# Kernel optimization log

Measured on AMD Instinct MI355X. Metric: run time of the kernel, lower is better.

The kernel has to match this reference:

```python
import jax, jax.numpy as jnp
import numpy as np

N, D, H, HD, R, K, TM = 32768, 128, 2, 64, 2, 32, 2
E_EDGES, M_MOTIFS, NG = 262144, 131072, 32
EPS = 1e-5
BETA_MAX = 5.0
GRAD_CLIP = 1.0
STATE_CLIP = 10.0
DAMPING = 1.0

def _isp(x):
    # inverse softplus of init values (params stored pre-softplus)
    return float(np.log(np.expm1(x)))

LAM2_RAW, LAM3_RAW, LAMM_RAW = _isp(1.0), _isp(0.5), _isp(1.0)
B2_RAW, B3_RAW, BM_RAW = _isp(1.0), _isp(1.0), _isp(1.0)


def layernorm(x, g, b):
    mu = x.mean(-1, keepdims=True)
    v = ((x - mu) ** 2).mean(-1, keepdims=True)
    return g * (x - mu) * jax.lax.rsqrt(v + EPS) + b


def seg_lse(s, seg, n, beta):
    # tempered logsumexp over segments: (1/beta) log sum_j exp(beta*s_j); s:[items,H] -> [n,H]
    sb = beta * s
    m = jax.ops.segment_max(sb, seg, num_segments=n)
    m = jnp.where(jnp.isfinite(m), m, 0.0)
    z = jax.ops.segment_sum(jnp.exp(sb - m[seg]), seg, num_segments=n)
    return jnp.where(z > 0, (m + jnp.log(jnp.maximum(z, 1e-30))) / beta, 0.0)


def energy(X, a_2, ln_gamma, ln_beta, W_Q2, W_K2, W_Q3, W_K3, T_tau, W_Qm, W_Km, B_mem,
           c_2, u_2, c_3, u_3, v_3, t_tau, batch):
    sp = jax.nn.softplus
    lam2, lam3, lamm = sp(LAM2_RAW), sp(LAM3_RAW), sp(LAMM_RAW)
    b2 = jnp.minimum(sp(B2_RAW), BETA_MAX)
    b3 = jnp.minimum(sp(B3_RAW), BETA_MAX)
    bm = jnp.minimum(sp(BM_RAW), BETA_MAX)
    G = layernorm(X, ln_gamma, ln_beta)
    # pairwise Q2/K2 term over edges (c_2 <- u_2) with learned per-edge bias a_2
    Q2 = jnp.einsum('nd,hzd->nhz', G, W_Q2)  # [N,H,HD]
    K2 = jnp.einsum('nd,hzd->nhz', G, W_K2)
    s2 = jnp.einsum('ehz,ehz->eh', Q2[c_2], K2[u_2]) / np.sqrt(HD) + a_2  # [E,H]
    e_pair = -lam2 * seg_lse(s2, c_2, N, b2).sum(-1)  # [N]
    # rank-R bilinear motif term over (c_3,u_3,v_3) with type embedding T_tau
    Q3 = jnp.einsum('nd,hzd->nhz', G, W_Q3).reshape(N, H, R, HD)
    K3 = jnp.einsum('nd,hzd->nhz', G, W_K3).reshape(N, H, R, HD)
    qk = jnp.einsum('mhrz,mhrz->mhr', Q3[c_3], K3[u_3])
    tv = jnp.einsum('mhrz,mhrz->mhr', T_tau[t_tau], K3[v_3])
    s3 = (qk * tv).sum(-1) / HD  # [M,H]
    e_motif = -lam3 * seg_lse(s3, c_3, N, b3).sum(-1)
    # K-slot memory term
    Qm = jnp.einsum('nd,hzd->nhz', G, W_Qm)
    Km = jnp.einsum('kd,hzd->hkz', B_mem, W_Km)
    sm = jnp.einsum('nhz,hkz->nhk', Qm, Km) / np.sqrt(HD)
    e_mem = -(lamm / bm) * jax.nn.logsumexp(bm * sm, axis=-1).sum(-1)
    e_node = 0.5 * (X * X).sum(-1) + e_pair + e_motif + e_mem
    return jax.ops.segment_sum(e_node, batch, num_segments=NG)  # per-graph energy [NG]


def setup_inputs() -> dict:
    key = jax.random.key(0)
    ks = jax.random.split(key, 16)
    inp = {}
    inp['X'] = jax.random.normal(ks[0], (N, D), jnp.float32)
    inp['c_2'] = jax.random.randint(ks[1], (E_EDGES,), 0, N)
    inp['u_2'] = jax.random.randint(ks[2], (E_EDGES,), 0, N)
    inp['c_3'] = jax.random.randint(ks[3], (M_MOTIFS,), 0, N)
    inp['u_3'] = jax.random.randint(ks[4], (M_MOTIFS,), 0, N)
    inp['v_3'] = jax.random.randint(ks[5], (M_MOTIFS,), 0, N)
    inp['t_tau'] = jax.random.randint(ks[6], (M_MOTIFS,), 0, TM)
    inp['batch'] = jnp.sort(jax.random.randint(ks[7], (N,), 0, NG))
    inp['a_2'] = 0.1 * jax.random.normal(ks[8], (E_EDGES, H), jnp.float32)
    inp['step_size'] = jnp.full((1,), 0.1, jnp.float32)
    inp['ln_gamma'] = jnp.ones((D,), jnp.float32)
    inp['ln_beta'] = jnp.zeros((D,), jnp.float32)
    s = 1.0 / np.sqrt(D)
    inp['W_Q2'] = s * jax.random.normal(ks[9], (H, HD, D), jnp.float32)
    inp['W_K2'] = s * jax.random.normal(ks[10], (H, HD, D), jnp.float32)
    inp['W_Q3'] = 0.5 * s * jax.random.normal(ks[11], (H, R * HD, D), jnp.float32)
    inp['W_K3'] = 0.5 * s * jax.random.normal(ks[12], (H, R * HD, D), jnp.float32)
    inp['T_tau'] = 0.02 * jax.random.normal(ks[13], (TM, H, R, HD), jnp.float32)
    inp['W_Qm'] = 0.5 * s * jax.random.normal(ks[14], (H, HD, D), jnp.float32)
    inp['W_Km'] = 0.5 * s * jax.random.normal(ks[15], (H, HD, D), jnp.float32)
    inp['B_mem'] = s * jax.random.normal(jax.random.fold_in(key, 99), (K, D), jnp.float32)
    return inp


def reference(X, c_2, u_2, c_3, u_3, v_3, t_tau, batch, a_2, step_size,
              ln_gamma, ln_beta, W_Q2, W_K2, W_Q3, W_K3, T_tau, W_Qm, W_Km, B_mem):
    Eg, vjp = jax.vjp(
        lambda Xv: energy(Xv, a_2, ln_gamma, ln_beta, W_Q2, W_K2, W_Q3, W_K3, T_tau,
                          W_Qm, W_Km, B_mem, c_2, u_2, c_3, u_3, v_3, t_tau, batch), X)
    gX, = vjp(jnp.ones_like(Eg))
    gnorm = jnp.linalg.norm(gX, axis=-1, keepdims=True)
    gX = gX * (GRAD_CLIP / jnp.maximum(gnorm, GRAD_CLIP))
    X_next = X - step_size[0] * DAMPING * gX
    snorm = jnp.linalg.norm(X_next, axis=-1, keepdims=True)
    X_next = X_next * (STATE_CLIP / jnp.maximum(snorm, STATE_CLIP))
    return X_next, Eg
```

## Files before the change

kernel.cpp:

```cpp
#include <hip/hip_runtime.h>
#include <hip/hip_bf16.h>
#include <math.h>

typedef __hip_bfloat16 bf16;
typedef short bf16x8 __attribute__((ext_vector_type(8)));
typedef float f32x4 __attribute__((ext_vector_type(4)));

#define N_NODES 32768
#define D_DIM 128
#define E_EDG 262144
#define M_MOT 131072
#define NG_G 32
#define F_TOT 832

__device__ __forceinline__ float wsum64(float v){
#pragma unroll
  for (int o = 32; o > 0; o >>= 1) v += __shfl_xor(v, o, 64);
  return v;
}
__device__ __forceinline__ float hsum32(float v){
#pragma unroll
  for (int o = 16; o > 0; o >>= 1) v += __shfl_xor(v, o, 64);
  return v;
}
__device__ __forceinline__ float hmax32(float v){
#pragma unroll
  for (int o = 16; o > 0; o >>= 1) v = fmaxf(v, __shfl_xor(v, o, 64));
  return v;
}
__device__ __forceinline__ float hsum16(float v){
#pragma unroll
  for (int o = 8; o > 0; o >>= 1) v += __shfl_xor(v, o, 64);
  return v;
}
__device__ __forceinline__ float hsum8(float v){
#pragma unroll
  for (int o = 4; o > 0; o >>= 1) v += __shfl_xor(v, o, 64);
  return v;
}
__device__ __forceinline__ float bsum128(float v, float* scr, int t){
  float s = wsum64(v);
  if ((t & 63) == 0) scr[t >> 6] = s;
  __syncthreads();
  float r = scr[0] + scr[1];
  __syncthreads();
  return r;
}
__device__ __forceinline__ float bflo(unsigned u){ return __uint_as_float(u << 16); }
__device__ __forceinline__ float bfhi(unsigned u){ return __uint_as_float(u & 0xffff0000u); }
__device__ __forceinline__ unsigned packbf(float x, float y){
  bf16 a = __float2bfloat16(x), b = __float2bfloat16(y);
  unsigned short ua = *(unsigned short*)&a, ub = *(unsigned short*)&b;
  return (unsigned)ua | ((unsigned)ub << 16);
}
__device__ __forceinline__ void unpk8(uint4 p, float* f){
  f[0] = bflo(p.x); f[1] = bfhi(p.x); f[2] = bflo(p.y); f[3] = bfhi(p.y);
  f[4] = bflo(p.z); f[5] = bfhi(p.z); f[6] = bflo(p.w); f[7] = bfhi(p.w);
}

__global__ __launch_bounds__(256) void k_phaseA(
    const int* c2, const int* u2, const int* c3, const int* u3, const int* v3,
    const float* wq2, const float* wk2, const float* wq3, const float* wk3,
    const float* wqm, const float* wkm, const float* bmem, const float* Ttau,
    int* cnt, float* Wcat, bf16* Ttb, float* Mprod){
  __shared__ float KmL[64];
  int b = blockIdx.x, t = threadIdx.x;
  if (b < 1024){
    int i = b * 256 + t;
    atomicAdd(&cnt[c2[i]], 1);
    atomicAdd(&cnt[N_NODES + u2[i]], 1);
    if (i < M_MOT){
      atomicAdd(&cnt[2 * N_NODES + c3[i]], 1);
      atomicAdd(&cnt[3 * N_NODES + u3[i]], 1);
      atomicAdd(&cnt[4 * N_NODES + v3[i]], 1);
    }
  } else if (b < 1440){
    int idx = (b - 1024) * 256 + t;
    if (idx < 768 * D_DIM){
      int f = idx / D_DIM, d = idx - f * D_DIM;
      const float* src; int fr;
      if      (f < 128){ src = wq2; fr = f; }
      else if (f < 256){ src = wk2; fr = f - 128; }
      else if (f < 512){ src = wq3; fr = f - 256; }
      else             { src = wk3; fr = f - 512; }
      Wcat[f * D_DIM + d] = src[fr * D_DIM + d];
    } else {
      int j = idx - 768 * D_DIM;
      Ttb[j] = __float2bfloat16(Ttau[j]);
    }
  } else {
    int hk = b - 1440;
    int h = hk >> 5, k = hk & 31;
    if (t < 64){
      const float* wrow = wkm + (size_t)(h * 64 + t) * D_DIM;
      const float* brow = bmem + k * D_DIM;
      float acc = 0.f;
      for (int d = 0; d < D_DIM; d++) acc += wrow[d] * brow[d];
      KmL[t] = acc;
    }
    __syncthreads();
    if (t < 128){
      const float* w = wqm + (size_t)(h * 64) * 128 + t;
      float acc = 0.f;
      for (int z = 0; z < 64; z++) acc += w[z * 128] * KmL[z];
      Mprod[t * 64 + hk] = acc;
    }
  }
}

__global__ __launch_bounds__(1024) void k_phaseB(
    int* cntcur, int* off,
    const float* X, const float* gamma, const float* beta,
    bf16* Gb, float* mu, float* rstd, float* e_node,
    const float* Wcat, const float* Mprod, bf16* wfF, bf16* wfB){
  __shared__ int sd[1024];
  int b = blockIdx.x, t = threadIdx.x;
  if (b < 5){
    int a = b;
    int* c = cntcur + a * N_NODES;
    int* o = off + a * (N_NODES + 1);
    int loc[32];
    int sum = 0;
#pragma unroll
    for (int j = 0; j < 32; j++){ loc[j] = sum; sum += c[t * 32 + j]; }
    sd[t] = sum;
    __syncthreads();
    for (int s = 1; s < 1024; s <<= 1){
      int v = (t >= s) ? sd[t - s] : 0;
      __syncthreads();
      sd[t] += v;
      __syncthreads();
    }
    int excl = sd[t] - sum;
#pragma unroll
    for (int j = 0; j < 32; j++){
      int val = excl + loc[j];
      o[t * 32 + j] = val;
      c[t * 32 + j] = val;
    }
    if (t == 1023) o[N_NODES] = sd[1023];
  } else if (b < 2053){
    int wv = t >> 6, l = t & 63;
    int n = (b - 5) * 16 + wv;
    float2 x2 = ((const float2*)(X + (size_t)n * 128))[l];
    float sumx = wsum64(x2.x + x2.y);
    float sumxx = wsum64(x2.x * x2.x + x2.y * x2.y);
    float m = sumx * (1.0f / 128.0f);
    float var = sumxx * (1.0f / 128.0f) - m * m;
    float rs = rsqrtf(var + 1e-5f);
    float2 gg = ((const float2*)gamma)[l];
    float2 bb = ((const float2*)beta)[l];
    ((unsigned*)(Gb + (size_t)n * 128))[l] =
        packbf(gg.x * (x2.x - m) * rs + bb.x, gg.y * (x2.y - m) * rs + bb.y);
    if (l == 0){ mu[n] = m; rstd[n] = rs; e_node[n] = 0.5f * sumxx; }
  } else {
    int idx = (b - 2053) * 1024 + t;
    int j = idx & 7, lane = (idx >> 3) & 63, tt = idx >> 9;
    {
      int tn = tt >> 2, kt = tt & 3;
      int f = tn * 16 + (lane & 15), d = kt * 32 + (lane >> 4) * 8 + j;
      float v = (f < 768) ? Wcat[f * 128 + d] : 0.125f * Mprod[d * 64 + (f - 768)];
      wfF[idx] = __float2bfloat16(v);
    }
    {
      int td = tt / 26, tf = tt - td * 26;
      int f = tf * 32 + (lane >> 4) * 8 + j, d = td * 16 + (lane & 15);
      float v = (f < 768) ? Wcat[f * 128 + d] : -0.125f * Mprod[d * 64 + (f - 768)];
      wfB[idx] = __float2bfloat16(v);
    }
  }
}

__global__ __launch_bounds__(256) void k_phaseC(
    const bf16* Gb, const bf16* wfF, bf16* P,
    const int* c2, const int* u2, const int* c3, const int* u3, const int* v3,
    const int* tt, const float* a2, int* cur,
    uint2* lec, uint2* leu, uint2* lmc, uint2* lmu, uint2* lmv){
  int b = blockIdx.x;
  int g = b / 15, r = b - g * 15;
  if (r < 13){
    int f = g * 13 + r;
    int bx = f & 511, by = f >> 9;
    int wave = threadIdx.x >> 6, lane = threadIdx.x & 63;
    int m0 = bx * 64 + wave * 16;
    int tn0 = by * 4;
    int rw = lane & 15, quad = lane >> 4;
    const bf16* aptr = Gb + (size_t)(m0 + rw) * 128 + quad * 8;
    bf16x8 a[4];
#pragma unroll
    for (int kt = 0; kt < 4; kt++) a[kt] = *(const bf16x8*)(aptr + kt * 32);
    f32x4 acc[4];
#pragma unroll
    for (int i = 0; i < 4; i++) acc[i] = (f32x4){0.f, 0.f, 0.f, 0.f};
#pragma unroll
    for (int nf = 0; nf < 4; nf++){
      int tn = tn0 + nf;
#pragma unroll
      for (int kt = 0; kt < 4; kt++){
        bf16x8 bb = *(const bf16x8*)(wfF + (((size_t)tn * 4 + kt) * 64 + lane) * 8);
        acc[nf] = __builtin_amdgcn_mfma_f32_16x16x32_bf16(a[kt], bb, acc[nf], 0, 0, 0);
      }
    }
#pragma unroll
    for (int nf = 0; nf < 4; nf++){
      int col = (tn0 + nf) * 16 + rw;
#pragma unroll
      for (int rr = 0; rr < 4; rr++){
        int row = m0 + quad * 4 + rr;
        P[(size_t)row * F_TOT + col] = __float2bfloat16(acc[nf][rr]);
      }
    }
  } else {
    int i = (g * 2 + (r - 13)) * 256 + threadIdx.x;
    {
      int c = c2[i], u = u2[i];
      int posc = atomicAdd(&cur[c], 1);
      float2 av = *(const float2*)(a2 + (size_t)i * 2);
      lec[posc] = make_uint2((unsigned)u, packbf(av.x, av.y));
      int posu = atomicAdd(&cur[N_NODES + u], 1);
      leu[posu] = make_uint2((unsigned)c, (unsigned)posc);
    }
    if (i < M_MOT){
      int c = c3[i], u = u3[i], v = v3[i], t = tt[i];
      int posc = atomicAdd(&cur[2 * N_NODES + c], 1);
      lmc[posc] = make_uint2((unsigned)(u | (v << 16)), (unsigned)t);
      int posu = atomicAdd(&cur[3 * N_NODES + u], 1);
      lmu[posu] = make_uint2((unsigned)c, (unsigned)posc);
      int posv = atomicAdd(&cur[4 * N_NODES + v], 1);
      lmv[posv] = make_uint2((unsigned)(c | (t << 16)), (unsigned)posc);
    }
  }
}

__global__ __launch_bounds__(256) void k_fused_c(const bf16* P, const uint2* lec, const uint2* lmc,
                   const bf16* Ttb, const int* off_ec, const int* off_mc,
                   float* s2, float* rz2, float* s3, float* qkb, float* tvb, float* rz3,
                   bf16* dP, float* e_pair, float* e_mot, float* e_mem){
  int b = blockIdx.x;
  int type = b % 3, grp = b / 3;
  int wave = threadIdx.x >> 6, z = threadIdx.x & 63;
  int n = grp * 4 + wave;
  int l = z & 31, lh = z >> 5;

  if (type == 0){
    int hg = l >> 4;
    int beg = off_ec[n], end = off_ec[n + 1];
    uint2 qp = ((const uint2*)(P + (size_t)n * F_TOT))[l];
    float q0 = bflo(qp.x), q1 = bfhi(qp.x), q2 = bflo(qp.y), q3 = bfhi(qp.y);
    float a0 = 0.f, a1 = 0.f, a2 = 0.f, a3 = 0.f, zz = 0.f;
    int iters = (end - beg + 1) >> 1;
    for (int it = 0; it < iters; it++){
      int idx = beg + 2 * it + lh;
      bool valid = idx < end;
      int idc = valid ? idx : end - 1;
      uint2 pl = lec[idc];
      uint2 kp = ((const uint2*)(P + (size_t)pl.x * F_TOT + 128))[l];
      float k0 = bflo(kp.x), k1 = bfhi(kp.x), k2 = bflo(kp.y), k3 = bfhi(kp.y);
      float s = hsum16(q0 * k0 + q1 * k1 + q2 * k2 + q3 * k3) * 0.125f
              + (hg ? bfhi(pl.y) : bflo(pl.y));
      if (valid && (l & 15) == 0) s2[2 * idx + hg] = s;
      float ex = valid ? expf(s) : 0.f;
      a0 += ex * k0;  a1 += ex * k1;  a2 += ex * k2;  a3 += ex * k3;
      zz += ex;
    }
    a0 += __shfl_xor(a0, 32, 64);  a1 += __shfl_xor(a1, 32, 64);
    a2 += __shfl_xor(a2, 32, 64);  a3 += __shfl_xor(a3, 32, 64);
    zz += __shfl_xor(zz, 32, 64);
    float rz = (zz > 0.f) ? 1.0f / zz : 0.f;
    float coef = -0.125f * rz;
    if (z < 32){
      uint2 o;
      o.x = packbf(coef * a0, coef * a1);
      o.y = packbf(coef * a2, coef * a3);
      ((uint2*)(dP + (size_t)n * F_TOT))[l] = o;
      if ((l & 15) == 0) rz2[n * 2 + hg] = rz;
    }
    float eterm = (zz > 0.f) ? -logf(zz) : 0.f;
    float eo = __shfl(eterm, 16, 64);
    if (z == 0) e_pair[n] = eterm + eo;
  } else if (type == 1){
    int g = l >> 3, hg = g >> 1;
    int beg = off_mc[n], end = off_mc[n + 1];
    uint4 qp = ((const uint4*)(P + (size_t)n * F_TOT + 256))[l];
    float q[8]; unpk8(qp, q);
    float acc[8] = {0,0,0,0,0,0,0,0};
    float zz = 0.f;
    int iters = (end - beg + 1) >> 1;
    for (int it = 0; it < iters; it++){
      int idx = beg + 2 * it + lh;
      bool valid = idx < end;
      int idc = valid ? idx : end - 1;
      uint2 pl = lmc[idc];
      int u = pl.x & 0xffff, v = pl.x >> 16, t = pl.y;
      uint4 kup = ((const uint4*)(P + (size_t)u * F_TOT + 512))[l];
      uint4 kvp = ((const uint4*)(P + (size_t)v * F_TOT + 512))[l];
      uint4 tp  = ((const uint4*)(Ttb + (size_t)t * 256))[l];
      float k[8], vv[8], pt[8];
      unpk8(kup, k); unpk8(kvp, vv); unpk8(tp, pt);
      float dq = 0.f, dt = 0.f;
#pragma unroll
      for (int j = 0; j < 8; j++){ dq += q[j] * k[j]; dt += pt[j] * vv[j]; }
      float qk = hsum8(dq);
      float tv = hsum8(dt);
      if (valid && (l & 7) == 0){ qkb[(size_t)4 * idx + g] = qk; tvb[(size_t)4 * idx + g] = tv; }
      float w = qk * tv;
      float s = (w + __shfl_xor(w, 8, 64)) * (1.0f / 64.0f);
      if (valid && (l & 15) == 0) s3[2 * idx + hg] = s;
      float ex = valid ? expf(s) : 0.f;
      float et = ex * tv;
#pragma unroll
      for (int j = 0; j < 8; j++) acc[j] += et * k[j];
      zz += ex;
    }
#pragma unroll
    for (int j = 0; j < 8; j++) acc[j] += __shfl_xor(acc[j], 32, 64);
    zz += __shfl_xor(zz, 32, 64);
    float rz = (zz > 0.f) ? 1.0f / zz : 0.f;
    float coef = (-0.5f / 64.0f) * rz;
    if (z < 32){
      uint4 o;
      o.x = packbf(coef * acc[0], coef * acc[1]);
      o.y = packbf(coef * acc[2], coef * acc[3]);
      o.z = packbf(coef * acc[4], coef * acc[5]);
      o.w = packbf(coef * acc[6], coef * acc[7]);
      ((uint4*)(dP + (size_t)n * F_TOT + 256))[l] = o;
      if ((l & 15) == 0) rz3[n * 2 + hg] = rz;
    }
    float eterm = (zz > 0.f) ? -0.5f * logf(zz) : 0.f;
    float eo = __shfl(eterm, 16, 64);
    if (z == 0) e_mot[n] = eterm + eo;
  } else {
    unsigned short us = ((const unsigned short*)(P + (size_t)n * F_TOT + 768))[z];
    float s = __uint_as_float((unsigned)us << 16);
    float mx = hmax32(s);
    float ex = expf(s - mx);
    float se = hsum32(ex);
    float p = ex / se;
    bf16 pb = __float2bfloat16(p);
    ((unsigned short*)(dP + (size_t)n * F_TOT + 768))[z] = *(unsigned short*)&pb;
    float eterm = -(mx + logf(se));
    float eo = __shfl(eterm, z ^ 32, 64);
    if (z == 0) e_mem[n] = eterm + eo;
  }
}

__global__ __launch_bounds__(256) void k_phaseE(const bf16* P, const uint2* leu,
                    const uint2* lmu, const uint2* lmv, const bf16* Ttb,
                    const float* s2, const float* rz2, const float* s3, const float* rz3,
                    const float* qkb, const float* tvb,
                    const int* off_eu, const int* off_mu, const int* off_mv, bf16* dP,
                    const float* e_node, const float* e_pair, const float* e_mot,
                    const float* e_mem, const int* batch, float* Eg){
  __shared__ float eg[NG_G];
  int b = blockIdx.x;
  if (b < 128){
    int t = threadIdx.x;
    if (t < NG_G) eg[t] = 0.f;
    __syncthreads();
    int n = b * 256 + t;
    float e = e_node[n] + e_pair[n] + e_mot[n] + e_mem[n];
    atomicAdd(&eg[batch[n]], e);
    __syncthreads();
    if (t < NG_G) atomicAdd(&Eg[t], eg[t]);
    return;
  }
  int b2 = b - 128;
  int type = b2 & 1, grp = b2 >> 1;
  int wave = threadIdx.x >> 6, z = threadIdx.x & 63;
  int n = grp * 4 + wave;
  int l = z & 31, lh = z >> 5;

  if (type == 0){
    int hg = l >> 4;
    int beg = off_eu[n], end = off_eu[n + 1];
    float a0 = 0.f, a1 = 0.f, a2 = 0.f, a3 = 0.f;
    int iters = (end - beg + 1) >> 1;
    for (int it = 0; it < iters; it++){
      int idx = beg + 2 * it + lh;
      bool valid = idx < end;
      int idc = valid ? idx : end - 1;
      uint2 pl = leu[idc];
      uint2 qp = ((const uint2*)(P + (size_t)pl.x * F_TOT))[l];
      float p = valid ? expf(s2[2 * pl.y + hg]) * rz2[pl.x * 2 + hg] : 0.f;
      a0 += p * bflo(qp.x);  a1 += p * bfhi(qp.x);
      a2 += p * bflo(qp.y);  a3 += p * bfhi(qp.y);
    }
    a0 += __shfl_xor(a0, 32, 64);  a1 += __shfl_xor(a1, 32, 64);
    a2 += __shfl_xor(a2, 32, 64);  a3 += __shfl_xor(a3, 32, 64);
    if (z < 32){
      uint2 o;
      o.x = packbf(-0.125f * a0, -0.125f * a1);
      o.y = packbf(-0.125f * a2, -0.125f * a3);
      ((uint2*)(dP + (size_t)n * F_TOT + 128))[l] = o;
    }
  } else {
    int g = l >> 3, hg = g >> 1;
    float acc[8] = {0,0,0,0,0,0,0,0};
    {
      int beg = off_mu[n], end = off_mu[n + 1];
      int iters = (end - beg + 1) >> 1;
      for (int it = 0; it < iters; it++){
        int idx = beg + 2 * it + lh;
        bool valid = idx < end;
        int idc = valid ? idx : end - 1;
        uint2 pl = lmu[idc];
        unsigned c = pl.x, posc = pl.y;
        uint4 qp = ((const uint4*)(P + (size_t)c * F_TOT + 256))[l];
        float q[8]; unpk8(qp, q);
        float w = valid ? expf(s3[2 * posc + hg]) * rz3[c * 2 + hg] * tvb[(size_t)4 * posc + g] : 0.f;
#pragma unroll
        for (int j = 0; j < 8; j++) acc[j] += w * q[j];
      }
    }
    {
      int beg = off_mv[n], end = off_mv[n + 1];
      int iters = (end - beg + 1) >> 1;
      for (int it = 0; it < iters; it++){
        int idx = beg + 2 * it + lh;
        bool valid = idx < end;
        int idc = valid ? idx : end - 1;
        uint2 pl = lmv[idc];
        unsigned c = pl.x & 0xffff, t = pl.x >> 16, posc = pl.y;
        uint4 tp = ((const uint4*)(Ttb + (size_t)t * 256))[l];
        float pt[8]; unpk8(tp, pt);
        float w = valid ? expf(s3[2 * posc + hg]) * rz3[c * 2 + hg] * qkb[(size_t)4 * posc + g] : 0.f;
#pragma unroll
        for (int j = 0; j < 8; j++) acc[j] += w * pt[j];
      }
    }
#pragma unroll
    for (int j = 0; j < 8; j++) acc[j] += __shfl_xor(acc[j], 32, 64);
    const float cst = -0.5f / 64.0f;
    if (z < 32){
      uint4 o;
      o.x = packbf(cst * acc[0], cst * acc[1]);
      o.y = packbf(cst * acc[2], cst * acc[3]);
      o.z = packbf(cst * acc[4], cst * acc[5]);
      o.w = packbf(cst * acc[6], cst * acc[7]);
      ((uint4*)(dP + (size_t)n * F_TOT + 512))[l] = o;
    }
  }
}

__global__ __launch_bounds__(256) void k_bwd_mfma(const bf16* dP, const bf16* wfB, float* dG){
  int wave = threadIdx.x >> 6, lane = threadIdx.x & 63;
  int m0 = blockIdx.x * 64 + wave * 16;
  int rw = lane & 15, quad = lane >> 4;
  const bf16* aptr = dP + (size_t)(m0 + rw) * F_TOT + quad * 8;
  f32x4 acc[8];
#pragma unroll
  for (int i = 0; i < 8; i++) acc[i] = (f32x4){0.f, 0.f, 0.f, 0.f};
  for (int kt = 0; kt < 26; kt++){
    bf16x8 a = *(const bf16x8*)(aptr + kt * 32);
#pragma unroll
    for (int td = 0; td < 8; td++){
      bf16x8 b = *(const bf16x8*)(wfB + (((size_t)td * 26 + kt) * 64 + lane) * 8);
      acc[td] = __builtin_amdgcn_mfma_f32_16x16x32_bf16(a, b, acc[td], 0, 0, 0);
    }
  }
#pragma unroll
  for (int td = 0; td < 8; td++){
    int col = td * 16 + rw;
#pragma unroll
    for (int r = 0; r < 4; r++){
      int row = m0 + quad * 4 + r;
      dG[(size_t)row * 128 + col] = acc[td][r];
    }
  }
}

__global__ __launch_bounds__(128) void k_finalize(const float* X, const float* dG, const float* gamma,
                    const float* mu, const float* rstd, const float* step_p,
                    const float* Eg, float* out){
  __shared__ float scr[2];
  int n = blockIdx.x, t = threadIdx.x;
  float x = X[(size_t)n * 128 + t];
  float dg = dG[(size_t)n * 128 + t];
  float gam = gamma[t];
  float rs = rstd[n];
  float xhat = (x - mu[n]) * rs;
  float dxh = dg * gam;
  float s1 = bsum128(dxh, scr, t);
  float s2v = bsum128(dxh * xhat, scr, t);
  float dx = rs * (dxh - s1 * (1.0f / 128) - xhat * (s2v * (1.0f / 128)));
  float g = x + dx;
  float gn = sqrtf(bsum128(g * g, scr, t));
  g *= 1.0f / fmaxf(gn, 1.0f);
  float step = step_p[0];
  float xn = x - step * g;
  float sn = sqrtf(bsum128(xn * xn, scr, t));
  xn *= 10.0f / fmaxf(sn, 10.0f);
  out[(size_t)n * 128 + t] = xn;
  if (n == 0 && t < NG_G) out[(size_t)N_NODES * 128 + t] = Eg[t];
}

extern "C" void kernel_launch(void* const* d_in, const int* in_sizes, int n_in,
                              void* d_out, int out_size, void* d_ws, size_t ws_size,
                              hipStream_t stream) {
  const float* X     = (const float*)d_in[0];
  const int*  c_2    = (const int*) d_in[1];
  const int*  u_2    = (const int*) d_in[2];
  const int*  c_3    = (const int*) d_in[3];
  const int*  u_3    = (const int*) d_in[4];
  const int*  v_3    = (const int*) d_in[5];
  const int*  t_tau  = (const int*) d_in[6];
  const int*  batch  = (const int*) d_in[7];
  const float* a_2   = (const float*)d_in[8];
  const float* step_s= (const float*)d_in[9];
  const float* ln_g  = (const float*)d_in[10];
  const float* ln_b  = (const float*)d_in[11];
  const float* W_Q2  = (const float*)d_in[12];
  const float* W_K2  = (const float*)d_in[13];
  const float* W_Q3  = (const float*)d_in[14];
  const float* W_K3  = (const float*)d_in[15];
  const float* T_tau = (const float*)d_in[16];
  const float* W_Qm  = (const float*)d_in[17];
  const float* W_Km  = (const float*)d_in[18];
  const float* B_mem = (const float*)d_in[19];
  float* out = (float*)d_out;

  char* wb = (char*)d_ws;
  float* Wcat   = (float*)wb; wb += 768 * D_DIM * 4;
  float* Mprod  = (float*)wb; wb += 8192 * 4;
  float* mu     = (float*)wb; wb += N_NODES * 4;
  float* rstd   = (float*)wb; wb += N_NODES * 4;
  float* s2     = (float*)wb; wb += (size_t)E_EDG * 2 * 4;
  float* rz2    = (float*)wb; wb += N_NODES * 2 * 4;
  float* s3     = (float*)wb; wb += (size_t)M_MOT * 2 * 4;
  float* qkb    = (float*)wb; wb += (size_t)M_MOT * 4 * 4;
  float* tvb    = (float*)wb; wb += (size_t)M_MOT * 4 * 4;
  float* rz3    = (float*)wb; wb += N_NODES * 2 * 4;
  float* e_node = (float*)wb; wb += N_NODES * 4;
  float* e_pair = (float*)wb; wb += N_NODES * 4;
  float* e_mot  = (float*)wb; wb += N_NODES * 4;
  float* e_mem  = (float*)wb; wb += N_NODES * 4;
  float* Eg     = (float*)wb; wb += NG_G * 4;
  float* dG     = (float*)wb; wb += (size_t)N_NODES * D_DIM * 4;
  bf16* Gb      = (bf16*)wb;  wb += (size_t)N_NODES * D_DIM * 2;
  bf16* P       = (bf16*)wb;  wb += (size_t)N_NODES * F_TOT * 2;
  bf16* dP      = (bf16*)wb;  wb += (size_t)N_NODES * F_TOT * 2;
  bf16* wfF     = (bf16*)wb;  wb += 106496 * 2;
  bf16* wfB     = (bf16*)wb;  wb += 106496 * 2;
  bf16* Ttb     = (bf16*)wb;  wb += 8192 * 2;
  int* cntcur   = (int*)wb;   wb += 5 * N_NODES * 4;
  int* off      = (int*)wb;   wb += 5 * (N_NODES + 1) * 4;
  wb = (char*)(((size_t)wb + 15) & ~(size_t)15);
  uint2* lec    = (uint2*)wb; wb += (size_t)E_EDG * 8;
  uint2* leu    = (uint2*)wb; wb += (size_t)E_EDG * 8;
  uint2* lmc    = (uint2*)wb; wb += (size_t)M_MOT * 8;
  uint2* lmu    = (uint2*)wb; wb += (size_t)M_MOT * 8;
  uint2* lmv    = (uint2*)wb; wb += (size_t)M_MOT * 8;

  const int* off_ec = off;
  const int* off_eu = off + (N_NODES + 1);
  const int* off_mc = off + 2 * (N_NODES + 1);
  const int* off_mu = off + 3 * (N_NODES + 1);
  const int* off_mv = off + 4 * (N_NODES + 1);

  hipMemsetAsync(cntcur, 0, 5 * N_NODES * sizeof(int), stream);
  hipMemsetAsync(Eg, 0, NG_G * sizeof(float), stream);
  hipLaunchKernelGGL(k_phaseA, dim3(1504), dim3(256), 0, stream,
                     c_2, u_2, c_3, u_3, v_3, W_Q2, W_K2, W_Q3, W_K3,
                     W_Qm, W_Km, B_mem, T_tau, cntcur, Wcat, Ttb, Mprod);
  hipLaunchKernelGGL(k_phaseB, dim3(2157), dim3(1024), 0, stream,
                     cntcur, off, X, ln_g, ln_b, Gb, mu, rstd, e_node,
                     Wcat, Mprod, wfF, wfB);
  hipLaunchKernelGGL(k_phaseC, dim3(7680), dim3(256), 0, stream,
                     Gb, wfF, P, c_2, u_2, c_3, u_3, v_3, t_tau, a_2, cntcur,
                     lec, leu, lmc, lmu, lmv);
  hipLaunchKernelGGL(k_fused_c, dim3(3 * (N_NODES / 4)), dim3(256), 0, stream,
                     P, lec, lmc, Ttb, off_ec, off_mc,
                     s2, rz2, s3, qkb, tvb, rz3, dP, e_pair, e_mot, e_mem);
  hipLaunchKernelGGL(k_phaseE, dim3(128 + 2 * (N_NODES / 4)), dim3(256), 0, stream,
                     P, leu, lmu, lmv, Ttb, s2, rz2, s3, rz3, qkb, tvb,
                     off_eu, off_mu, off_mv, dP,
                     e_node, e_pair, e_mot, e_mem, batch, Eg);
  hipLaunchKernelGGL(k_bwd_mfma, dim3(N_NODES / 64), dim3(256), 0, stream, dP, wfB, dG);
  hipLaunchKernelGGL(k_finalize, dim3(N_NODES), dim3(128), 0, stream,
                     X, dG, ln_g, mu, rstd, step_s, Eg, out);
}
```

Measured before the change: 395.2 us.

## Split backward GEMM by K-tiles, overlap part with phaseE, widen pair gathers

The backward MFMA GEMM is split into two K-tile masks. Tiles whose dP rows are already final after k_fused_c are computed inside k_phaseE, running alongside the scatter work, and the remaining tiles run in a second accumulating kernel. The pair-edge loops in k_fused_c and k_phaseE now process four edges per wave with 16-byte gathers instead of two edges with 8-byte gathers. k_finalize packs four nodes per block with wave-only reductions, removing the shared-memory block syncs. The risks are the extra read-modify-write of dG in the second GEMM pass and correctness depending on the hand-coded tile masks matching which dP columns each phase writes.

Measured after the change: 459.7 us. 1.16x slower.

```diff
diff --git a/kernel.cpp b/kernel.cpp
--- a/kernel.cpp
+++ b/kernel.cpp
@@ -12,6 +12,8 @@
 #define M_MOT 131072
 #define NG_G 32
 #define F_TOT 832
+#define BWD_MASK1 0x0300FF0Fu
+#define BWD_MASK2 0x00FF00F0u
 
 __device__ __forceinline__ float wsum64(float v){
 #pragma unroll
@@ -28,23 +30,10 @@
   for (int o = 16; o > 0; o >>= 1) v = fmaxf(v, __shfl_xor(v, o, 64));
   return v;
 }
-__device__ __forceinline__ float hsum16(float v){
-#pragma unroll
-  for (int o = 8; o > 0; o >>= 1) v += __shfl_xor(v, o, 64);
-  return v;
-}
 __device__ __forceinline__ float hsum8(float v){
 #pragma unroll
   for (int o = 4; o > 0; o >>= 1) v += __shfl_xor(v, o, 64);
   return v;
-}
-__device__ __forceinline__ float bsum128(float v, float* scr, int t){
-  float s = wsum64(v);
-  if ((t & 63) == 0) scr[t >> 6] = s;
-  __syncthreads();
-  float r = scr[0] + scr[1];
-  __syncthreads();
-  return r;
 }
 __device__ __forceinline__ float bflo(unsigned u){ return __uint_as_float(u << 16); }
 __device__ __forceinline__ float bfhi(unsigned u){ return __uint_as_float(u & 0xffff0000u); }
@@ -56,6 +45,36 @@
 __device__ __forceinline__ void unpk8(uint4 p, float* f){
   f[0] = bflo(p.x); f[1] = bfhi(p.x); f[2] = bflo(p.y); f[3] = bfhi(p.y);
   f[4] = bflo(p.z); f[5] = bfhi(p.z); f[6] = bflo(p.w); f[7] = bfhi(p.w);
+}
+
+__device__ __forceinline__ void bwd_body(const bf16* dP, const bf16* wfB, float* dG,
+                                         unsigned mask, bool accum, int b, int tid){
+  int wave = tid >> 6, lane = tid & 63;
+  int m0 = b * 64 + wave * 16;
+  int rw = lane & 15, quad = lane >> 4;
+  const bf16* aptr = dP + (size_t)(m0 + rw) * F_TOT + quad * 8;
+  f32x4 acc[8];
+#pragma unroll
+  for (int i = 0; i < 8; i++) acc[i] = (f32x4){0.f, 0.f, 0.f, 0.f};
+  for (int kt = 0; kt < 26; kt++){
+    if (!((mask >> kt) & 1u)) continue;
+    bf16x8 a = *(const bf16x8*)(aptr + kt * 32);
+#pragma unroll
+    for (int td = 0; td < 8; td++){
+      bf16x8 bb = *(const bf16x8*)(wfB + (((size_t)td * 26 + kt) * 64 + lane) * 8);
+      acc[td] = __builtin_amdgcn_mfma_f32_16x16x32_bf16(a, bb, acc[td], 0, 0, 0);
+    }
+  }
+#pragma unroll
+  for (int td = 0; td < 8; td++){
+    int col = td * 16 + rw;
+#pragma unroll
+    for (int r = 0; r < 4; r++){
+      int row = m0 + quad * 4 + r;
+      if (accum) dG[(size_t)row * 128 + col] += acc[td][r];
+      else       dG[(size_t)row * 128 + col]  = acc[td][r];
+    }
+  }
 }
 
 __global__ __launch_bounds__(256) void k_phaseA(
@@ -243,46 +262,56 @@
   int l = z & 31, lh = z >> 5;
 
   if (type == 0){
-    int hg = l >> 4;
+    int q = z >> 4, l16 = z & 15, hg = l16 >> 3;
     int beg = off_ec[n], end = off_ec[n + 1];
-    uint2 qp = ((const uint2*)(P + (size_t)n * F_TOT))[l];
-    float q0 = bflo(qp.x), q1 = bfhi(qp.x), q2 = bflo(qp.y), q3 = bfhi(qp.y);
-    float a0 = 0.f, a1 = 0.f, a2 = 0.f, a3 = 0.f, zz = 0.f;
-    int iters = (end - beg + 1) >> 1;
+    uint4 qp = ((const uint4*)(P + (size_t)n * F_TOT))[l16];
+    float qv[8]; unpk8(qp, qv);
+    float acc[8] = {0,0,0,0,0,0,0,0};
+    float zz = 0.f;
+    int iters = (end - beg + 3) >> 2;
     for (int it = 0; it < iters; it++){
-      int idx = beg + 2 * it + lh;
+      int idx = beg + 4 * it + q;
       bool valid = idx < end;
       int idc = valid ? idx : end - 1;
       uint2 pl = lec[idc];
-      uint2 kp = ((const uint2*)(P + (size_t)pl.x * F_TOT + 128))[l];
-      float k0 = bflo(kp.x), k1 = bfhi(kp.x), k2 = bflo(kp.y), k3 = bfhi(kp.y);
-      float s = hsum16(q0 * k0 + q1 * k1 + q2 * k2 + q3 * k3) * 0.125f
-              + (hg ? bfhi(pl.y) : bflo(pl.y));
-      if (valid && (l & 15) == 0) s2[2 * idx + hg] = s;
+      uint4 kp = ((const uint4*)(P + (size_t)pl.x * F_TOT + 128))[l16];
+      float kv[8]; unpk8(kp, kv);
+      float d = 0.f;
+#pragma unroll
+      for (int j = 0; j < 8; j++) d += qv[j] * kv[j];
+      float s = hsum8(d) * 0.125f + (hg ? bfhi(pl.y) : bflo(pl.y));
+      if (valid && (l16 & 7) == 0) s2[2 * idx + hg] = s;
       float ex = valid ? expf(s) : 0.f;
-      a0 += ex * k0;  a1 += ex * k1;  a2 += ex * k2;  a3 += ex * k3;
+#pragma unroll
+      for (int j = 0; j < 8; j++) acc[j] += ex * kv[j];
       zz += ex;
     }
-    a0 += __shfl_xor(a0, 32, 64);  a1 += __shfl_xor(a1, 32, 64);
-    a2 += __shfl_xor(a2, 32, 64);  a3 += __shfl_xor(a3, 32, 64);
+#pragma unroll
+    for (int j = 0; j < 8; j++){
+      acc[j] += __shfl_xor(acc[j], 16, 64);
+      acc[j] += __shfl_xor(acc[j], 32, 64);
+    }
+    zz += __shfl_xor(zz, 16, 64);
     zz += __shfl_xor(zz, 32, 64);
     float rz = (zz > 0.f) ? 1.0f / zz : 0.f;
     float coef = -0.125f * rz;
-    if (z < 32){
-      uint2 o;
-      o.x = packbf(coef * a0, coef * a1);
-      o.y = packbf(coef * a2, coef * a3);
-      ((uint2*)(dP + (size_t)n * F_TOT))[l] = o;
-      if ((l & 15) == 0) rz2[n * 2 + hg] = rz;
+    if (z < 16){
+      uint4 o;
+      o.x = packbf(coef * acc[0], coef * acc[1]);
+      o.y = packbf(coef * acc[2], coef * acc[3]);
+      o.z = packbf(coef * acc[4], coef * acc[5]);
+      o.w = packbf(coef * acc[6], coef * acc[7]);
+      ((uint4*)(dP + (size_t)n * F_TOT))[l16] = o;
+      if ((l16 & 7) == 0) rz2[n * 2 + hg] = rz;
     }
     float eterm = (zz > 0.f) ? -logf(zz) : 0.f;
-    float eo = __shfl(eterm, 16, 64);
+    float eo = __shfl(eterm, 8, 64);
     if (z == 0) e_pair[n] = eterm + eo;
   } else if (type == 1){
     int g = l >> 3, hg = g >> 1;
     int beg = off_mc[n], end = off_mc[n + 1];
     uint4 qp = ((const uint4*)(P + (size_t)n * F_TOT + 256))[l];
-    float q[8]; unpk8(qp, q);
+    float qv[8]; unpk8(qp, qv);
     float acc[8] = {0,0,0,0,0,0,0,0};
     float zz = 0.f;
     int iters = (end - beg + 1) >> 1;
@@ -299,7 +328,7 @@
       unpk8(kup, k); unpk8(kvp, vv); unpk8(tp, pt);
       float dq = 0.f, dt = 0.f;
 #pragma unroll
-      for (int j = 0; j < 8; j++){ dq += q[j] * k[j]; dt += pt[j] * vv[j]; }
+      for (int j = 0; j < 8; j++){ dq += qv[j] * k[j]; dt += pt[j] * vv[j]; }
       float qk = hsum8(dq);
       float tv = hsum8(dt);
       if (valid && (l & 7) == 0){ qkb[(size_t)4 * idx + g] = qk; tvb[(size_t)4 * idx + g] = tv; }
@@ -350,48 +379,59 @@
                     const float* qkb, const float* tvb,
                     const int* off_eu, const int* off_mu, const int* off_mv, bf16* dP,
                     const float* e_node, const float* e_pair, const float* e_mot,
-                    const float* e_mem, const int* batch, float* Eg){
+                    const float* e_mem, const int* batch, float* Eg,
+                    const bf16* wfB, float* dG){
   __shared__ float eg[NG_G];
   int b = blockIdx.x;
-  if (b < 128){
+  if (b < 512){
+    bwd_body(dP, wfB, dG, BWD_MASK1, false, b, threadIdx.x);
+    return;
+  }
+  if (b < 640){
     int t = threadIdx.x;
     if (t < NG_G) eg[t] = 0.f;
     __syncthreads();
-    int n = b * 256 + t;
+    int n = (b - 512) * 256 + t;
     float e = e_node[n] + e_pair[n] + e_mot[n] + e_mem[n];
     atomicAdd(&eg[batch[n]], e);
     __syncthreads();
     if (t < NG_G) atomicAdd(&Eg[t], eg[t]);
     return;
   }
-  int b2 = b - 128;
+  int b2 = b - 640;
   int type = b2 & 1, grp = b2 >> 1;
   int wave = threadIdx.x >> 6, z = threadIdx.x & 63;
   int n = grp * 4 + wave;
   int l = z & 31, lh = z >> 5;
 
   if (type == 0){
-    int hg = l >> 4;
+    int q = z >> 4, l16 = z & 15, hg = l16 >> 3;
     int beg = off_eu[n], end = off_eu[n + 1];
-    float a0 = 0.f, a1 = 0.f, a2 = 0.f, a3 = 0.f;
-    int iters = (end - beg + 1) >> 1;
+    float acc[8] = {0,0,0,0,0,0,0,0};
+    int iters = (end - beg + 3) >> 2;
     for (int it = 0; it < iters; it++){
-      int idx = beg + 2 * it + lh;
+      int idx = beg + 4 * it + q;
       bool valid = idx < end;
       int idc = valid ? idx : end - 1;
       uint2 pl = leu[idc];
-      uint2 qp = ((const uint2*)(P + (size_t)pl.x * F_TOT))[l];
+      uint4 qp = ((const uint4*)(P + (size_t)pl.x * F_TOT))[l16];
+      float qv[8]; unpk8(qp, qv);
       float p = valid ? expf(s2[2 * pl.y + hg]) * rz2[pl.x * 2 + hg] : 0.f;
-      a0 += p * bflo(qp.x);  a1 += p * bfhi(qp.x);
-      a2 += p * bflo(qp.y);  a3 += p * bfhi(qp.y);
-    }
-    a0 += __shfl_xor(a0, 32, 64);  a1 += __shfl_xor(a1, 32, 64);
-    a2 += __shfl_xor(a2, 32, 64);  a3 += __shfl_xor(a3, 32, 64);
-    if (z < 32){
-      uint2 o;
-      o.x = packbf(-0.125f * a0, -0.125f * a1);
-      o.y = packbf(-0.125f * a2, -0.125f * a3);
-      ((uint2*)(dP + (size_t)n * F_TOT + 128))[l] = o;
+#pragma unroll
+      for (int j = 0; j < 8; j++) acc[j] += p * qv[j];
+    }
+#pragma unroll
+    for (int j = 0; j < 8; j++){
+      acc[j] += __shfl_xor(acc[j], 16, 64);
+      acc[j] += __shfl_xor(acc[j], 32, 64);
+    }
+    if (z < 16){
+      uint4 o;
+      o.x = packbf(-0.125f * acc[0], -0.125f * acc[1]);
+      o.y = packbf(-0.125f * acc[2], -0.125f * acc[3]);
+      o.z = packbf(-0.125f * acc[4], -0.125f * acc[5]);
+      o.w = packbf(-0.125f * acc[6], -0.125f * acc[7]);
+      ((uint4*)(dP + (size_t)n * F_TOT + 128))[l16] = o;
     }
   } else {
     int g = l >> 3, hg = g >> 1;
@@ -406,10 +446,10 @@
         uint2 pl = lmu[idc];
         unsigned c = pl.x, posc = pl.y;
         uint4 qp = ((const uint4*)(P + (size_t)c * F_TOT + 256))[l];
-        float q[8]; unpk8(qp, q);
+        float qv[8]; unpk8(qp, qv);
         float w = valid ? expf(s3[2 * posc + hg]) * rz3[c * 2 + hg] * tvb[(size_t)4 * posc + g] : 0.f;
 #pragma unroll
-        for (int j = 0; j < 8; j++) acc[j] += w * q[j];
+        for (int j = 0; j < 8; j++) acc[j] += w * qv[j];
       }
     }
     {
@@ -442,56 +482,35 @@
   }
 }
 
-__global__ __launch_bounds__(256) void k_bwd_mfma(const bf16* dP, const bf16* wfB, float* dG){
-  int wave = threadIdx.x >> 6, lane = threadIdx.x & 63;
-  int m0 = blockIdx.x * 64 + wave * 16;
-  int rw = lane & 15, quad = lane >> 4;
-  const bf16* aptr = dP + (size_t)(m0 + rw) * F_TOT + quad * 8;
-  f32x4 acc[8];
-#pragma unroll
-  for (int i = 0; i < 8; i++) acc[i] = (f32x4){0.f, 0.f, 0.f, 0.f};
-  for (int kt = 0; kt < 26; kt++){
-    bf16x8 a = *(const bf16x8*)(aptr + kt * 32);
-#pragma unroll
-    for (int td = 0; td < 8; td++){
-      bf16x8 b = *(const bf16x8*)(wfB + (((size_t)td * 26 + kt) * 64 + lane) * 8);
-      acc[td] = __builtin_amdgcn_mfma_f32_16x16x32_bf16(a, b, acc[td], 0, 0, 0);
-    }
-  }
-#pragma unroll
-  for (int td = 0; td < 8; td++){
-    int col = td * 16 + rw;
-#pragma unroll
-    for (int r = 0; r < 4; r++){
-      int row = m0 + quad * 4 + r;
-      dG[(size_t)row * 128 + col] = acc[td][r];
-    }
-  }
-}
-
-__global__ __launch_bounds__(128) void k_finalize(const float* X, const float* dG, const float* gamma,
+__global__ __launch_bounds__(256) void k_bwd2(const bf16* dP, const bf16* wfB, float* dG){
+  bwd_body(dP, wfB, dG, BWD_MASK2, true, blockIdx.x, threadIdx.x);
+}
+
+__global__ __launch_bounds__(256) void k_finalize(const float* X, const float* dG, const float* gamma,
                     const float* mu, const float* rstd, const float* step_p,
                     const float* Eg, float* out){
-  __shared__ float scr[2];
-  int n = blockIdx.x, t = threadIdx.x;
-  float x = X[(size_t)n * 128 + t];
-  float dg = dG[(size_t)n * 128 + t];
-  float gam = gamma[t];
-  float rs = rstd[n];
-  float xhat = (x - mu[n]) * rs;
-  float dxh = dg * gam;
-  float s1 = bsum128(dxh, scr, t);
-  float s2v = bsum128(dxh * xhat, scr, t);
-  float dx = rs * (dxh - s1 * (1.0f / 128) - xhat * (s2v * (1.0f / 128)));
-  float g = x + dx;
-  float gn = sqrtf(bsum128(g * g, scr, t));
-  g *= 1.0f / fmaxf(gn, 1.0f);
+  int wave = threadIdx.x >> 6, l = threadIdx.x & 63;
+  int n = blockIdx.x * 4 + wave;
+  float2 x2 = ((const float2*)(X + (size_t)n * 128))[l];
+  float2 dg2 = ((const float2*)(dG + (size_t)n * 128))[l];
+  float2 gg = ((const float2*)gamma)[l];
+  float rs = rstd[n], m = mu[n];
+  float xh0 = (x2.x - m) * rs, xh1 = (x2.y - m) * rs;
+  float dxh0 = dg2.x * gg.x, dxh1 = dg2.y * gg.y;
+  float s1 = wsum64(dxh0 + dxh1);
+  float s2v = wsum64(dxh0 * xh0 + dxh1 * xh1);
+  float g0 = x2.x + rs * (dxh0 - s1 * (1.0f / 128) - xh0 * (s2v * (1.0f / 128)));
+  float g1 = x2.y + rs * (dxh1 - s1 * (1.0f / 128) - xh1 * (s2v * (1.0f / 128)));
+  float gn = sqrtf(wsum64(g0 * g0 + g1 * g1));
+  float gc = 1.0f / fmaxf(gn, 1.0f);
+  g0 *= gc; g1 *= gc;
   float step = step_p[0];
-  float xn = x - step * g;
-  float sn = sqrtf(bsum128(xn * xn, scr, t));
-  xn *= 10.0f / fmaxf(sn, 10.0f);
-  out[(size_t)n * 128 + t] = xn;
-  if (n == 0 && t < NG_G) out[(size_t)N_NODES * 128 + t] = Eg[t];
+  float xn0 = x2.x - step * g0, xn1 = x2.y - step * g1;
+  float sn = sqrtf(wsum64(xn0 * xn0 + xn1 * xn1));
+  float sc = 10.0f / fmaxf(sn, 10.0f);
+  ((float2*)(out + (size_t)n * 128))[l] = make_float2(xn0 * sc, xn1 * sc);
+  if (blockIdx.x == 0 && threadIdx.x < NG_G)
+    out[(size_t)N_NODES * 128 + threadIdx.x] = Eg[threadIdx.x];
 }
 
 extern "C" void kernel_launch(void* const* d_in, const int* in_sizes, int n_in,
@@ -571,11 +590,11 @@
   hipLaunchKernelGGL(k_fused_c, dim3(3 * (N_NODES / 4)), dim3(256), 0, stream,
                      P, lec, lmc, Ttb, off_ec, off_mc,
                      s2, rz2, s3, qkb, tvb, rz3, dP, e_pair, e_mot, e_mem);
-  hipLaunchKernelGGL(k_phaseE, dim3(128 + 2 * (N_NODES / 4)), dim3(256), 0, stream,
+  hipLaunchKernelGGL(k_phaseE, dim3(640 + 2 * (N_NODES / 4)), dim3(256), 0, stream,
                      P, leu, lmu, lmv, Ttb, s2, rz2, s3, rz3, qkb, tvb,
                      off_eu, off_mu, off_mv, dP,
-                     e_node, e_pair, e_mot, e_mem, batch, Eg);
-  hipLaunchKernelGGL(k_bwd_mfma, dim3(N_NODES / 64), dim3(256), 0, stream, dP, wfB, dG);
-  hipLaunchKernelGGL(k_finalize, dim3(N_NODES), dim3(128), 0, stream,
+                     e_node, e_pair, e_mot, e_mem, batch, Eg, wfB, dG);
+  hipLaunchKernelGGL(k_bwd2, dim3(N_NODES / 64), dim3(256), 0, stream, dP, wfB, dG);
+  hipLaunchKernelGGL(k_finalize, dim3(N_NODES / 4), dim3(256), 0, stream,
                      X, dG, ln_g, mu, rstd, step_s, Eg, out);
 }
```
